# Optimization experiments

Measured on AMD Instinct MI355X. Metric: run time of the kernel, lower is better.

Reference implementation:

```python
import jax, jax.numpy as jnp
import numpy as np

BATCH, NUM_BSS, NUM_USERS, M, N = 32, 8, 32, 128, 4
LAGR_ITERS = 8
PSEUDOINV_SVAL_THRESH = 1e-12


def herm(a):
    return 0.5 * (a + jnp.swapaxes(a, -1, -2).conj())


def setup_inputs() -> dict:
    key = jax.random.key(0)
    ks = jax.random.split(key, 7)
    v_re = jax.random.normal(ks[0], (BATCH, NUM_USERS, M, N), jnp.float32)
    v_im = jax.random.normal(ks[1], (BATCH, NUM_USERS, M, N), jnp.float32)
    H_re = jax.random.normal(ks[2], (NUM_BSS, NUM_USERS, N, M), jnp.float32)
    H_im = jax.random.normal(ks[3], (NUM_BSS, NUM_USERS, N, M), jnp.float32)
    noise_pow = jax.random.uniform(ks[4], (BATCH, NUM_USERS), jnp.float32, 0.05, 1.0)
    rweights = jax.random.uniform(ks[5], (BATCH, NUM_USERS), jnp.float32, 0.1, 1.0)
    bss_pow = jnp.ones((BATCH, NUM_BSS), jnp.float32)
    assign = jax.random.randint(ks[6], (NUM_USERS,), 0, NUM_BSS).astype(jnp.int32)
    return {"v_re": v_re, "v_im": v_im, "H_re": H_re, "H_im": H_im,
            "noise_pow": noise_pow, "rweights": rweights, "bss_pow": bss_pow,
            "assign": assign}


def reference(v_re, v_im, H_re, H_im, noise_pow, rweights, bss_pow, assign):
    V = v_re + 1j * v_im          # [B,K,M,N] precoders
    H = H_re + 1j * H_im          # [C,K,N,M] channel BS c -> user k
    K = V.shape[1]
    C = H.shape[0]
    Ndim = V.shape[-1]
    eyeN = jnp.eye(Ndim, dtype=V.dtype)

    # Hg[j, i] = channel from assigned-BS-of-user-j to user i
    Hg = H[assign]                                    # [K,K,N,M]
    # downlink covariance per user i: noise*I + sum_j (H[bs_j,i] V_j)(.)^H
    HV = jnp.einsum('jinm,bjmp->bijnp', Hg, V)        # [B,Ki,Kj,N,N]
    cov = jnp.einsum('bijnp,bijqp->binq', HV, HV.conj())
    cov = herm(cov + noise_pow[..., None, None] * eyeN)
    icov = herm(jnp.linalg.inv(cov))                  # [B,K,N,N]

    idx = jnp.arange(K)
    Hd = Hg[idx, idx]                                 # [K,N,M] direct channels
    HdV = jnp.einsum('knm,bkmp->bknp', Hd, V)         # [B,K,N,N]
    u = jnp.einsum('bknq,bkqp->bknp', icov, HdV)      # receive filters
    w_inv = herm(eyeN - jnp.einsum('bkqn,bkqp->bknp', u.conj(), HdV))
    w = herm(jnp.linalg.inv(w_inv))                   # MSE weights (w_poly=None)
    uwu = herm(jnp.einsum('bknp,bkpq,bkrq->bknr', u, w, u.conj()))
    # v_tilde = H_ii^H u w * rate_weight
    vt = jnp.einsum('knm,bknp,bkpq->bkmq', Hd.conj(), u, w) * rweights[..., None, None]

    # uplink covariance per BS c: sum_k rw_k * H[c,k]^H uwu_k H[c,k]
    ul = herm(jnp.einsum('cknm,bkno,ckop,bk->bcmp', H.conj(), uwu, H, rweights))

    # aux per BS: sum over assigned users of v_tilde v_tilde^H
    Q = jnp.einsum('bkmn,bkpn->bkmp', vt, vt.conj())  # [B,K,M,M]
    aux = jnp.moveaxis(
        jax.ops.segment_sum(jnp.moveaxis(Q, 1, 0), assign, num_segments=C), 0, 1)  # [B,C,M,M]

    lam, E = jnp.linalg.eigh(ul)                      # [B,C,M], [B,C,M,M]
    lam = jnp.maximum(lam, 0.0)
    c = jnp.maximum(jnp.einsum('bcmi,bcmp,bcpi->bci', E.conj(), aux, E).real, 0.0)
    c = c / bss_pow[..., None]

    # solve sum_i c_i/(lam_i+mu)^2 = 1 for mu >= 0 by bisection in [0, sqrt(sum c)]
    hi = jnp.sqrt(jnp.sum(c, -1))
    lo = jnp.zeros_like(hi)
    for _ in range(LAGR_ITERS):
        mid = 0.5 * (lo + hi)
        f = jnp.sum(c / jnp.square(lam + mid[..., None] + 1e-20), -1)
        gt = f > 1.0
        lo = jnp.where(gt, mid, lo)
        hi = jnp.where(gt, hi, mid)
    mu = jnp.maximum(0.5 * (lo + hi), 0.0)            # [B,C]

    # pseudo-inverse of loaded UL covariance via its eigendecomposition
    lam_l = lam + mu[..., None]
    lam_l = jnp.where(lam_l < PSEUDOINV_SVAL_THRESH, 1e12, lam_l)
    inv_aug = herm(jnp.einsum('bcmi,bci,bcni->bcmn', E, 1.0 / lam_l, E.conj()))

    # v update: v_k = inv_aug[assign_k] @ v_tilde_k
    v_out = jnp.einsum('bkmp,bkpn->bkmn', inv_aug[:, assign], vt)  # [B,K,M,N]
    return v_out
```

## Files before the change

### kernel.cpp

```cpp
#include <hip/hip_runtime.h>

#define B_ 32
#define C_ 8
#define K_ 32
#define NCMAX 96
#define BSTR 129

__device__ __forceinline__ float2 cmul(float2 a, float2 b) {
  return make_float2(a.x*b.x - a.y*b.y, a.x*b.y + a.y*b.x);
}
__device__ __forceinline__ float2 cmulc(float2 a, float2 b) {
  return make_float2(a.x*b.x + a.y*b.y, a.y*b.x - a.x*b.y);
}
__device__ __forceinline__ float2 cadd(float2 a, float2 b){ return make_float2(a.x+b.x, a.y+b.y); }
__device__ __forceinline__ float2 csub(float2 a, float2 b){ return make_float2(a.x-b.x, a.y-b.y); }
__device__ __forceinline__ int SK(int r){ return r + ((r >> 3) << 1); }

template<int C>
__device__ __forceinline__ float dppadd(float x) {
  return x + __int_as_float(__builtin_amdgcn_update_dpp(
      0, __float_as_int(x), C, 0xF, 0xF, true));
}
__device__ __forceinline__ float bcast63(float x) {
  return __int_as_float(__builtin_amdgcn_readlane(__float_as_int(x), 63));
}
__device__ __forceinline__ float red4f(float x) {
  x = dppadd<0xB1>(x); return dppadd<0x4E>(x);
}
__device__ __forceinline__ float red16f(float x) {
  x = dppadd<0xB1>(x); x = dppadd<0x4E>(x);
  x = dppadd<0x141>(x); x = dppadd<0x140>(x);
  return x;
}
__device__ __forceinline__ float red64u(float x) {
  x = red16f(x);
  x = dppadd<0x142>(x);
  x = dppadd<0x143>(x);
  return bcast63(x);
}
__device__ __forceinline__ float2 red16c(float2 a){ a.x = red16f(a.x); a.y = red16f(a.y); return a; }
__device__ __forceinline__ float2 red64cu(float2 a){ a.x = red64u(a.x); a.y = red64u(a.y); return a; }

__device__ void herm4_inv(float2 a[4][4], float2 out[4][4]) {
  float idg[4];
  for (int j = 0; j < 4; ++j) {
    float d = sqrtf(fmaxf(a[j][j].x, 1e-30f));
    float id = 1.f / d;
    idg[j] = id;
    a[j][j] = make_float2(d, 0.f);
    for (int r = j+1; r < 4; ++r) { a[r][j].x *= id; a[r][j].y *= id; }
    for (int c = j+1; c < 4; ++c)
      for (int r = c; r < 4; ++r)
        a[r][c] = csub(a[r][c], cmulc(a[r][j], a[c][j]));
  }
  float2 li[4][4];
  for (int j = 0; j < 4; ++j) {
    li[j][j] = make_float2(idg[j], 0.f);
    for (int r = j+1; r < 4; ++r) {
      float2 s = make_float2(0.f, 0.f);
      for (int d = j; d < r; ++d) s = cadd(s, cmul(a[r][d], li[d][j]));
      li[r][j] = make_float2(-s.x*idg[r], -s.y*idg[r]);
    }
  }
  for (int p = 0; p < 4; ++p)
    for (int q = 0; q < 4; ++q) {
      float2 s = make_float2(0.f, 0.f);
      for (int d = (p > q ? p : q); d < 4; ++d)
        s = cadd(s, cmulc(li[d][q], li[d][p]));
      out[p][q] = s;
    }
}

__global__ __launch_bounds__(512, 1) void k_fused(
    const float* __restrict__ v_re, const float* __restrict__ v_im,
    const float* __restrict__ H_re, const float* __restrict__ H_im,
    const float* __restrict__ noise_pow, const float* __restrict__ rweights,
    const float* __restrict__ bss_pow, const int* __restrict__ assign_g,
    void* __restrict__ outp, int omode)
{
  const int t = threadIdx.x;
  const int lane = t & 63, wid = t >> 6;
  const int blk = blockIdx.x;
  const int b = blk >> 3, c = blk & 7;
  const int tm = t >> 4, tp = t & 15;
  const int rbase = tm * 4, cbase = tp * 8;

  __shared__ __align__(16) float2 BsL[NCMAX * BSTR];
  __shared__ __align__(16) float2 Arena[4224];
  __shared__ __align__(16) float2 pS[1024];
  __shared__ __align__(16) float2 wS[160];
  __shared__ __align__(16) float2 colS[160];
  __shared__ __align__(16) float2 pvS[128];
  __shared__ __align__(16) float2 tauS[128];
  __shared__ float dS[128], eS[128], cpS[128];
  __shared__ float red[8];
  __shared__ int asg[K_], ulist[K_], nc_s;

  float2* Wall = pS;
  float2* uwS  = pS + 512;
  float2* covS = Arena + 2576;
  float2* HdVS = Arena + 3088;
  float2* Tsc  = Arena;
  float2* Vp   = Arena;

  if (t < K_) asg[t] = assign_g[t];
  if (t == 0) {
    int n2 = 0;
    for (int k = 0; k < K_; ++k) if (assign_g[k] == c) ulist[n2++] = k;
    nc_s = n2;
  }
  {
    const int k = t >> 4, n = (t >> 2) & 3, q = t & 3;
    covS[t] = make_float2((n == q) ? noise_pow[b*K_ + k] : 0.f, 0.f);
  }
  __syncthreads();
  const int nc = nc_s;
  if (nc == 0) return;
  const int cols = 4 * nc;
  const int passes = (cols + 31) >> 5;

  {
    const int pn = t >> 2, qt = t & 3;
    const int kk = pn >> 2, nn = pn & 3;
    float2* Tb0 = Arena + 1552;
    float2* Tb1 = Arena + 2064;
    for (int j = 0; j < K_; j += 2) {
      #pragma unroll
      for (int bf = 0; bf < 2; ++bf) {
        const int vb = (b*K_ + j + bf) * 512;
        Arena[bf*776 + (t >> 2)*6 + (t & 3) + (t >> 7)*2] =
            make_float2(v_re[vb + t], v_im[vb + t]);
      }
      __syncthreads();
      float2 rr[2][4];
      #pragma unroll
      for (int bf = 0; bf < 2; ++bf) {
        const float2* Vq = Arena + bf*776 + qt*2;
        const int hb = ((asg[j + bf]*K_ + kk)*4 + nn) * 128;
        float2 a0 = {0,0}, a1 = {0,0}, a2 = {0,0}, a3 = {0,0};
        for (int m4 = qt*32; m4 < qt*32 + 32; m4 += 4) {
          const float4 hre = *(const float4*)&H_re[hb + m4];
          const float4 him = *(const float4*)&H_im[hb + m4];
          const float hx[4] = {hre.x, hre.y, hre.z, hre.w};
          const float hy[4] = {him.x, him.y, him.z, him.w};
          #pragma unroll
          for (int i2 = 0; i2 < 4; ++i2) {
            const float4 v01 = *(const float4*)&Vq[(m4 + i2)*6];
            const float4 v23 = *(const float4*)&Vq[(m4 + i2)*6 + 2];
            a0.x += hx[i2]*v01.x - hy[i2]*v01.y; a0.y += hx[i2]*v01.y + hy[i2]*v01.x;
            a1.x += hx[i2]*v01.z - hy[i2]*v01.w; a1.y += hx[i2]*v01.w + hy[i2]*v01.z;
            a2.x += hx[i2]*v23.x - hy[i2]*v23.y; a2.y += hx[i2]*v23.y + hy[i2]*v23.x;
            a3.x += hx[i2]*v23.z - hy[i2]*v23.w; a3.y += hx[i2]*v23.w + hy[i2]*v23.z;
          }
        }
        rr[bf][0] = a0; rr[bf][1] = a1; rr[bf][2] = a2; rr[bf][3] = a3;
      }
      #pragma unroll
      for (int bf = 0; bf < 2; ++bf)
        #pragma unroll
        for (int p = 0; p < 4; ++p) {
          rr[bf][p].x = red4f(rr[bf][p].x);
          rr[bf][p].y = red4f(rr[bf][p].y);
        }
      if (qt == 0) {
        #pragma unroll
        for (int p = 0; p < 4; ++p) {
          Tb0[pn*4 + p] = rr[0][p];
          Tb1[pn*4 + p] = rr[1][p];
        }
      }
      __syncthreads();
      {
        const int k2 = t >> 4, n2 = (t >> 2) & 3, q2 = t & 3;
        float2 acc = covS[t];
        #pragma unroll
        for (int p = 0; p < 4; ++p)
          acc = cadd(acc, cmulc(Tb0[(k2*4 + n2)*4 + p], Tb0[(k2*4 + q2)*4 + p]));
        #pragma unroll
        for (int p = 0; p < 4; ++p)
          acc = cadd(acc, cmulc(Tb1[(k2*4 + n2)*4 + p], Tb1[(k2*4 + q2)*4 + p]));
        covS[t] = acc;
        if (k2 == j)     HdVS[k2*16 + n2*4 + q2] = Tb0[(k2*4 + n2)*4 + q2];
        if (k2 == j + 1) HdVS[k2*16 + n2*4 + q2] = Tb1[(k2*4 + n2)*4 + q2];
      }
      __syncthreads();
    }
  }

  if (t < K_) {
    const int k = t;
    float2 a[4][4], ic[4][4], hv[4][4], u[4][4], wi[4][4], w[4][4], uw[4][4], W[4][4];
    const float rwk = rweights[b*K_ + k];
    for (int r = 0; r < 4; ++r)
      for (int c2 = 0; c2 < 4; ++c2) a[r][c2] = covS[k*16 + r*4 + c2];
    herm4_inv(a, ic);
    for (int r = 0; r < 4; ++r)
      for (int c2 = 0; c2 < 4; ++c2) hv[r][c2] = HdVS[k*16 + r*4 + c2];
    for (int n = 0; n < 4; ++n)
      for (int p = 0; p < 4; ++p) {
        float2 s = {0,0};
        for (int q = 0; q < 4; ++q) s = cadd(s, cmul(ic[n][q], hv[q][p]));
        u[n][p] = s;
      }
    for (int n = 0; n < 4; ++n)
      for (int p = 0; p < 4; ++p) {
        float2 s = make_float2((n == p) ? 1.f : 0.f, 0.f);
        for (int q = 0; q < 4; ++q) s = csub(s, cmulc(hv[q][p], u[q][n]));
        wi[n][p] = s;
      }
    herm4_inv(wi, w);
    for (int n = 0; n < 4; ++n)
      for (int q = 0; q < 4; ++q) {
        float2 s = {0,0};
        for (int p = 0; p < 4; ++p) s = cadd(s, cmul(u[n][p], w[p][q]));
        uw[n][q] = s;
      }
    for (int n = 0; n < 4; ++n)
      for (int r = 0; r < 4; ++r) {
        float2 s = {0,0};
        for (int q = 0; q < 4; ++q) s = cadd(s, cmulc(uw[n][q], u[r][q]));
        W[n][r] = make_float2(s.x * rwk, s.y * rwk);
      }
    for (int n = 0; n < 4; ++n)
      for (int r = n; r < 4; ++r) {
        float2 x1 = W[n][r], x2 = W[r][n];
        float2 hm = make_float2(0.5f*(x1.x + x2.x), 0.5f*(x1.y - x2.y));
        W[n][r] = hm; W[r][n] = make_float2(hm.x, -hm.y);
      }
    for (int idx = 0; idx < 16; ++idx) {
      uwS[k*16 + idx]  = uw[idx >> 2][idx & 3];
      Wall[k*16 + idx] = W[idx >> 2][idx & 3];
    }
  }
  __syncthreads();

  float2 Areg[4][8];
  #pragma unroll
  for (int j = 0; j < 4; ++j)
    #pragma unroll
    for (int cc = 0; cc < 8; ++cc) Areg[j][cc] = make_float2(0.f, 0.f);
  for (int k = 0; k < K_; k += 2) {
    #pragma unroll
    for (int bf = 0; bf < 2; ++bf) {
      const int hb = (c*K_ + k + bf) * 512;
      Arena[bf*520 + (t >> 7)*130 + (t & 127)] = make_float2(H_re[hb + t], H_im[hb + t]);
    }
    __syncthreads();
    #pragma unroll
    for (int bf = 0; bf < 2; ++bf) {
      const int n = t >> 7, p = t & 127;
      const float2* HsB = Arena + bf*520;
      const int kb = (k + bf)*16 + n*4;
      float2 y = {0,0};
      #pragma unroll
      for (int o = 0; o < 4; ++o) y = cadd(y, cmul(Wall[kb + o], HsB[o*130 + p]));
      Arena[1040 + bf*640 + n*160 + p + ((p >> 3) << 1)] = y;
    }
    __syncthreads();
    #pragma unroll
    for (int bf = 0; bf < 2; ++bf) {
      const float2* HsB = Arena + bf*520;
      const float2* YsB = Arena + 1040 + bf*640;
      #pragma unroll
      for (int n = 0; n < 4; ++n) {
        const float4 ha = *(const float4*)&HsB[n*130 + rbase];
        const float4 hc = *(const float4*)&HsB[n*130 + rbase + 2];
        const float2 h0 = make_float2(ha.x, ha.y), h1 = make_float2(ha.z, ha.w);
        const float2 h2 = make_float2(hc.x, hc.y), h3 = make_float2(hc.z, hc.w);
        const float2* yb = &YsB[n*160 + tp*10];
        #pragma unroll
        for (int hq = 0; hq < 2; ++hq) {
          float2 y[4];
          #pragma unroll
          for (int a2 = 0; a2 < 4; a2 += 2) {
            const float4 y4 = *(const float4*)&yb[hq*4 + a2];
            y[a2] = make_float2(y4.x, y4.y); y[a2+1] = make_float2(y4.z, y4.w);
          }
          #pragma unroll
          for (int c4 = 0; c4 < 4; ++c4) {
            const int cc = hq*4 + c4;
            Areg[0][cc].x += h0.x*y[c4].x + h0.y*y[c4].y;
            Areg[0][cc].y += h0.x*y[c4].y - h0.y*y[c4].x;
            Areg[1][cc].x += h1.x*y[c4].x + h1.y*y[c4].y;
            Areg[1][cc].y += h1.x*y[c4].y - h1.y*y[c4].x;
            Areg[2][cc].x += h2.x*y[c4].x + h2.y*y[c4].y;
            Areg[2][cc].y += h2.x*y[c4].y - h2.y*y[c4].x;
            Areg[3][cc].x += h3.x*y[c4].x + h3.y*y[c4].y;
            Areg[3][cc].y += h3.x*y[c4].y - h3.y*y[c4].x;
          }
        }
      }
    }
    __syncthreads();
  }

  float2 Bw0[8], Bw1[8];
  #pragma unroll
  for (int qq = 0; qq < 8; ++qq) { Bw0[qq] = make_float2(0.f,0.f); Bw1[qq] = make_float2(0.f,0.f); }
  float trp = 0.f;
  #pragma unroll
  for (int qq = 0; qq < 8; ++qq) {
    const int col = wid + 8*qq;
    if (col < cols) {
      const int slot = col >> 2, qn = col & 3;
      const int k = ulist[slot];
      const float rwk = rweights[b*K_ + k];
      const int hb = (c*K_ + k) * 512;
      float2 a0 = {0,0}, a1 = {0,0};
      #pragma unroll
      for (int n = 0; n < 4; ++n) {
        const float2 uwv = uwS[k*16 + n*4 + qn];
        a0 = cadd(a0, cmulc(uwv, make_float2(H_re[hb + n*128 + lane],
                                             H_im[hb + n*128 + lane])));
        a1 = cadd(a1, cmulc(uwv, make_float2(H_re[hb + n*128 + lane + 64],
                                             H_im[hb + n*128 + lane + 64])));
      }
      a0.x *= rwk; a0.y *= rwk; a1.x *= rwk; a1.y *= rwk;
      Bw0[qq] = a0; Bw1[qq] = a1;
      trp += a0.x*a0.x + a0.y*a0.y + a1.x*a1.x + a1.y*a1.y;
    }
  }
  trp = red64u(trp);
  if (lane == 0) red[wid] = trp;
  __syncthreads();
  const float inv_bss = 1.f / bss_pow[b*C_ + c];
  float hi = sqrtf((red[0] + red[1] + red[2] + red[3] +
                    red[4] + red[5] + red[6] + red[7]) * inv_bss);
  float lo = 0.f;

  if (tp == 0) {
    #pragma unroll
    for (int j = 0; j < 4; ++j) colS[SK(rbase + j)] = Areg[j][0];
  }
  __syncthreads();

  #pragma unroll 1
  for (int i = 0; i < 127; ++i) {
    float2 vr[4], vc[8], v0, v1, tau, sc;
    {
      const float2 x0 = colS[SK(lane)], x1 = colS[SK(lane + 64)];
      float sig = 0.f;
      if (lane >= i + 2)      sig += x0.x*x0.x + x0.y*x0.y;
      if (lane + 64 >= i + 2) sig += x1.x*x1.x + x1.y*x1.y;
      sig = red64u(sig);
      const float2 al = colS[SK(i + 1)];
      float beta;
      if (sig <= 1e-30f && fabsf(al.y) <= 1e-30f) {
        beta = al.x; tau = make_float2(0.f, 0.f); sc = make_float2(0.f, 0.f);
      } else {
        const float mag = sqrtf(al.x*al.x + al.y*al.y + sig);
        beta = (al.x >= 0.f) ? -mag : mag;
        const float ib = 1.f / beta;
        tau = make_float2((beta - al.x) * ib, -al.y * ib);
        const float dx = al.x - beta, dy = al.y;
        const float dn = 1.f / (dx*dx + dy*dy);
        sc = make_float2(dx*dn, -dy*dn);
      }
      if (t == 0) { eS[i] = beta; tauS[i] = tau; }
      v0 = (lane <= i) ? make_float2(0.f,0.f)
         : (lane == i + 1 ? make_float2(1.f,0.f) : cmul(x0, sc));
      { const int r1 = lane + 64;
        v1 = (r1 <= i) ? make_float2(0.f,0.f)
           : (r1 == i + 1 ? make_float2(1.f,0.f) : cmul(x1, sc)); }
      #pragma unroll
      for (int j = 0; j < 4; ++j) {
        const int r = rbase + j;
        const float2 x = colS[SK(r)];
        vr[j] = (r <= i) ? make_float2(0.f, 0.f)
              : (r == i + 1 ? make_float2(1.f, 0.f) : cmul(x, sc));
      }
      {
        const int cb = SK(cbase);
        const float4 c01 = *(const float4*)&colS[cb];
        const float4 c23 = *(const float4*)&colS[cb + 2];
        const float4 c45 = *(const float4*)&colS[cb + 4];
        const float4 c67 = *(const float4*)&colS[cb + 6];
        const float2 cx[8] = { make_float2(c01.x,c01.y), make_float2(c01.z,c01.w),
                               make_float2(c23.x,c23.y), make_float2(c23.z,c23.w),
                               make_float2(c45.x,c45.y), make_float2(c45.z,c45.w),
                               make_float2(c67.x,c67.y), make_float2(c67.z,c67.w) };
        #pragma unroll
        for (int cc = 0; cc < 8; ++cc) {
          const int r = cbase + cc;
          vc[cc] = (r <= i) ? make_float2(0.f, 0.f)
                 : (r == i + 1 ? make_float2(1.f, 0.f) : cmul(cx[cc], sc));
        }
      }
    }
    {
      float2 part[4];
      #pragma unroll
      for (int j = 0; j < 4; ++j) {
        float2 s = cmul(Areg[j][0], vc[0]);
        #pragma unroll
        for (int cc = 1; cc < 8; ++cc) s = cadd(s, cmul(Areg[j][cc], vc[cc]));
        part[j] = s;
      }
      #pragma unroll
      for (int j = 0; j < 4; ++j) part[j] = red16c(part[j]);
      #pragma unroll
      for (int j = 0; j < 4; ++j) if (tp == j) pvS[rbase + j] = part[j];
      const float2 tauc = make_float2(tau.x, -tau.y);
      #pragma unroll
      for (int qq = 0; qq < 8; ++qq) {
        const int col = wid + 8*qq;
        if (col >= cols) continue;
        float2 d = cadd(cmulc(Bw0[qq], v0), cmulc(Bw1[qq], v1));
        d = red64cu(d);
        const float2 dBt = cmul(tauc, d);
        Bw0[qq] = csub(Bw0[qq], cmul(dBt, v0));
        Bw1[qq] = csub(Bw1[qq], cmul(dBt, v1));
      }
    }
    __syncthreads();

    if (wid == 0) {
      float2 p0 = {0.f,0.f}, p1 = {0.f,0.f};
      if (lane > i)      p0 = cmul(tau, pvS[lane]);
      if (lane + 64 > i) p1 = cmul(tau, pvS[lane + 64]);
      float2 d0 = cadd(cmulc(p0, v0), cmulc(p1, v1));
      d0 = red64cu(d0);
      const float alr = -0.5f * (tau.x*d0.x + tau.y*d0.y);
      wS[SK(lane)]      = cadd(p0, make_float2(alr*v0.x, alr*v0.y));
      wS[SK(lane + 64)] = cadd(p1, make_float2(alr*v1.x, alr*v1.y));
    }
    __syncthreads();

    {
      float2 wr[4], wc[8];
      #pragma unroll
      for (int j = 0; j < 4; ++j) wr[j] = wS[SK(rbase + j)];
      {
        const int cb = SK(cbase);
        const float4 w01 = *(const float4*)&wS[cb];
        const float4 w23 = *(const float4*)&wS[cb + 2];
        const float4 w45 = *(const float4*)&wS[cb + 4];
        const float4 w67 = *(const float4*)&wS[cb + 6];
        wc[0] = make_float2(w01.x,w01.y); wc[1] = make_float2(w01.z,w01.w);
        wc[2] = make_float2(w23.x,w23.y); wc[3] = make_float2(w23.z,w23.w);
        wc[4] = make_float2(w45.x,w45.y); wc[5] = make_float2(w45.z,w45.w);
        wc[6] = make_float2(w67.x,w67.y); wc[7] = make_float2(w67.z,w67.w);
      }
      #pragma unroll
      for (int j = 0; j < 4; ++j)
        #pragma unroll
        for (int cc = 0; cc < 8; ++cc)
          Areg[j][cc] = csub(Areg[j][cc], cadd(cmulc(vr[j], wc[cc]), cmulc(wr[j], vc[cc])));
      if (tp == (i >> 3)) {
        #pragma unroll
        for (int cc = 0; cc < 8; ++cc) if (cc == (i & 7)) {
          #pragma unroll
          for (int j = 0; j < 4; ++j) if (rbase + j >= i + 1) Areg[j][cc] = vr[j];
        }
      }
      if (tp == ((i + 1) >> 3)) {
        #pragma unroll
        for (int cc = 0; cc < 8; ++cc) if (cc == ((i + 1) & 7)) {
          #pragma unroll
          for (int j = 0; j < 4; ++j) colS[SK(rbase + j)] = Areg[j][cc];
        }
      }
    }
    __syncthreads();
  }

  if (tp == (tm >> 1)) {
    const int co = (tm & 1) * 4;
    #pragma unroll
    for (int j = 0; j < 4; ++j)
      #pragma unroll
      for (int cc = 0; cc < 8; ++cc)
        if (cc == co + j) dS[rbase + j] = Areg[j][cc].x;
  }
  #pragma unroll
  for (int qq = 0; qq < 8; ++qq) {
    const int col = wid + 8*qq;
    if (col < cols) {
      BsL[col*BSTR + lane]      = Bw0[qq];
      BsL[col*BSTR + lane + 64] = Bw1[qq];
    }
  }
  __syncthreads();

  if (wid == 0) {
    for (int it = 0; it <= 8; ++it) {
      const float mu = 0.5f * (lo + hi);
      float fsum = 0.f;
      for (int p = 0; p < passes; ++p) {
        const int colg = 32*p + (lane & 31);
        const bool act = (lane < 32) && (colg < cols);
        float2* Bcol = BsL + colg*BSTR;
        float m = dS[0] + mu;
        float im = 1.f / m;
        float2 g = act ? Bcol[0] : make_float2(0.f, 0.f);
        g.x *= im; g.y *= im;
        if (act) Tsc[lane] = g;
        float cp = eS[0] * im;
        if (lane == 0) cpS[0] = cp;
        #pragma unroll 4
        for (int r = 1; r < 128; ++r) {
          const float e0 = eS[r-1];
          m = dS[r] + mu - e0 * cp;
          im = 1.f / m;
          float2 gr = act ? Bcol[r] : make_float2(0.f, 0.f);
          gr.x = (gr.x - e0 * g.x) * im;
          gr.y = (gr.y - e0 * g.y) * im;
          g = gr;
          if (act) Tsc[r*33 + lane] = gr;
          if (r < 127) { cp = eS[r] * im; if (lane == 0) cpS[r] = cp; }
        }
        float2 z = g;
        float acc = z.x*z.x + z.y*z.y;
        if (it == 8 && act) Bcol[127] = z;
        #pragma unroll 4
        for (int r = 126; r >= 0; --r) {
          const float cpr = cpS[r];
          const float2 gp = act ? Tsc[r*33 + lane] : make_float2(0.f, 0.f);
          z.x = gp.x - cpr * z.x;
          z.y = gp.y - cpr * z.y;
          acc += z.x*z.x + z.y*z.y;
          if (it == 8 && act) Bcol[r] = z;
        }
        if (act) fsum += acc;
      }
      if (it < 8) {
        fsum = red64u(fsum);
        const float f = fsum * inv_bss;
        if (f > 1.0f) lo = mu; else hi = mu;
      }
    }
  }
  __syncthreads();

  for (int base = 0; base < cols; base += 32) {
    float2 z0[4], z1[4];
    bool act[4];
    #pragma unroll
    for (int qq = 0; qq < 4; ++qq) {
      const int col = base + wid + 8*qq;
      act[qq] = (col < cols);
      const int cc2 = act[qq] ? col : 0;
      z0[qq] = BsL[cc2*BSTR + lane];
      z1[qq] = BsL[cc2*BSTR + lane + 64];
    }
    for (int P = 7; P >= 0; --P) {
      const int p0i = P * 16;
      const int smax = (P == 7) ? 14 : 15;
      __syncthreads();
      if (tp == 2*P) {
        #pragma unroll
        for (int s = 0; s < 8; ++s) {
          const int ii = p0i + s;
          #pragma unroll
          for (int j = 0; j < 4; ++j) {
            const int r = rbase + j;
            Vp[(s << 7) + r] = (r >= ii + 1) ? Areg[j][s] : make_float2(0.f, 0.f);
          }
        }
      }
      if (tp == 2*P + 1) {
        #pragma unroll
        for (int s = 8; s < 16; ++s) {
          if (s > smax) continue;
          const int ii = p0i + s;
          #pragma unroll
          for (int j = 0; j < 4; ++j) {
            const int r = rbase + j;
            Vp[(s << 7) + r] = (r >= ii + 1) ? Areg[j][s - 8] : make_float2(0.f, 0.f);
          }
        }
      }
      __syncthreads();
      for (int s = smax; s >= 0; --s) {
        const float2 tv = tauS[p0i + s];
        const float2 v0b = Vp[(s << 7) + lane];
        const float2 v1b = Vp[(s << 7) + lane + 64];
        float2 d[4];
        #pragma unroll
        for (int qq = 0; qq < 4; ++qq) {
          d[qq] = cadd(cmulc(z0[qq], v0b), cmulc(z1[qq], v1b));
          d[qq] = red64cu(d[qq]);
        }
        #pragma unroll
        for (int qq = 0; qq < 4; ++qq) {
          const float2 td = cmul(tv, d[qq]);
          z0[qq] = csub(z0[qq], cmul(td, v0b));
          z1[qq] = csub(z1[qq], cmul(td, v1b));
        }
      }
    }
    #pragma unroll
    for (int qq = 0; qq < 4; ++qq) if (act[qq]) {
      const int col = base + wid + 8*qq;
      const int slotc = col >> 2, qn = col & 3;
      const int k = ulist[slotc];
      const size_t obase = (size_t)(b*K_ + k) * 512;
      const size_t oe0 = obase + (size_t)lane*4 + qn;
      const size_t oe1 = obase + (size_t)(lane + 64)*4 + qn;
      if (omode == 0) {
        ((float2*)outp)[oe0] = z0[qq];
        ((float2*)outp)[oe1] = z1[qq];
      } else {
        ((float*)outp)[oe0] = z0[qq].x;
        ((float*)outp)[oe1] = z1[qq].x;
      }
    }
  }
}

extern "C" void kernel_launch(void* const* d_in, const int* in_sizes, int n_in,
                              void* d_out, int out_size, void* d_ws, size_t ws_size,
                              hipStream_t stream)
{
  (void)in_sizes; (void)n_in; (void)d_ws; (void)ws_size;
  const float* v_re   = (const float*)d_in[0];
  const float* v_im   = (const float*)d_in[1];
  const float* H_re   = (const float*)d_in[2];
  const float* H_im   = (const float*)d_in[3];
  const float* noise  = (const float*)d_in[4];
  const float* rw     = (const float*)d_in[5];
  const float* bss    = (const float*)d_in[6];
  const int*   assign = (const int*)d_in[7];

  const int omode = (out_size == B_*K_*128*4) ? 1 : 0;

  hipLaunchKernelGGL(k_fused, dim3(B_*C_), dim3(512), 0, stream,
                     v_re, v_im, H_re, H_im, noise, rw, bss, assign, d_out, omode);
}
```

Measured before the change: 1.181 ms.

## Split tridiagonal bisection solves across two waves and drop w broadcast barrier

The bisection solve over batched tridiagonal systems now splits its column passes between two wavefronts instead of one. Each wave gets its own scratch (the second uses spare BsL space) and the waves combine partial sums through shared memory with barriers. In the Householder update loop, every thread now computes the w vector entries it needs from pvS, which removes one wS store and its __syncthreads per reflector step. The cost is redundant arithmetic per thread, extra barriers per bisection iteration, and a dependence on the BsL region past column 64 being free.

```diff
diff --git a/kernel.cpp b/kernel.cpp
--- a/kernel.cpp
+++ b/kernel.cpp
@@ -88,11 +88,10 @@
   __shared__ __align__(16) float2 BsL[NCMAX * BSTR];
   __shared__ __align__(16) float2 Arena[4224];
   __shared__ __align__(16) float2 pS[1024];
-  __shared__ __align__(16) float2 wS[160];
   __shared__ __align__(16) float2 colS[160];
-  __shared__ __align__(16) float2 pvS[128];
+  __shared__ __align__(16) float2 pvS[160];
   __shared__ __align__(16) float2 tauS[128];
-  __shared__ float dS[128], eS[128], cpS[128];
+  __shared__ float dS[128], eS[128], cpS[128], cpS2[128];
   __shared__ float red[8];
   __shared__ int asg[K_], ulist[K_], nc_s;
 
@@ -399,7 +398,7 @@
       #pragma unroll
       for (int j = 0; j < 4; ++j) part[j] = red16c(part[j]);
       #pragma unroll
-      for (int j = 0; j < 4; ++j) if (tp == j) pvS[rbase + j] = part[j];
+      for (int j = 0; j < 4; ++j) if (tp == j) pvS[SK(rbase + j)] = part[j];
       const float2 tauc = make_float2(tau.x, -tau.y);
       #pragma unroll
       for (int qq = 0; qq < 8; ++qq) {
@@ -414,38 +413,28 @@
     }
     __syncthreads();
 
-    if (wid == 0) {
-      float2 p0 = {0.f,0.f}, p1 = {0.f,0.f};
-      if (lane > i)      p0 = cmul(tau, pvS[lane]);
-      if (lane + 64 > i) p1 = cmul(tau, pvS[lane + 64]);
+    {
+      float2 p0 = (lane > i)      ? cmul(tau, pvS[SK(lane)])      : make_float2(0.f,0.f);
+      float2 p1 = (lane + 64 > i) ? cmul(tau, pvS[SK(lane + 64)]) : make_float2(0.f,0.f);
       float2 d0 = cadd(cmulc(p0, v0), cmulc(p1, v1));
       d0 = red64cu(d0);
       const float alr = -0.5f * (tau.x*d0.x + tau.y*d0.y);
-      wS[SK(lane)]      = cadd(p0, make_float2(alr*v0.x, alr*v0.y));
-      wS[SK(lane + 64)] = cadd(p1, make_float2(alr*v1.x, alr*v1.y));
-    }
-    __syncthreads();
-
-    {
-      float2 wr[4], wc[8];
-      #pragma unroll
-      for (int j = 0; j < 4; ++j) wr[j] = wS[SK(rbase + j)];
-      {
-        const int cb = SK(cbase);
-        const float4 w01 = *(const float4*)&wS[cb];
-        const float4 w23 = *(const float4*)&wS[cb + 2];
-        const float4 w45 = *(const float4*)&wS[cb + 4];
-        const float4 w67 = *(const float4*)&wS[cb + 6];
-        wc[0] = make_float2(w01.x,w01.y); wc[1] = make_float2(w01.z,w01.w);
-        wc[2] = make_float2(w23.x,w23.y); wc[3] = make_float2(w23.z,w23.w);
-        wc[4] = make_float2(w45.x,w45.y); wc[5] = make_float2(w45.z,w45.w);
-        wc[6] = make_float2(w67.x,w67.y); wc[7] = make_float2(w67.z,w67.w);
-      }
-      #pragma unroll
-      for (int j = 0; j < 4; ++j)
-        #pragma unroll
-        for (int cc = 0; cc < 8; ++cc)
-          Areg[j][cc] = csub(Areg[j][cc], cadd(cmulc(vr[j], wc[cc]), cmulc(wr[j], vc[cc])));
+      float2 wr[4];
+      #pragma unroll
+      for (int j = 0; j < 4; ++j) {
+        const int r = rbase + j;
+        float2 p = (r > i) ? cmul(tau, pvS[SK(r)]) : make_float2(0.f,0.f);
+        wr[j] = make_float2(p.x + alr*vr[j].x, p.y + alr*vr[j].y);
+      }
+      #pragma unroll
+      for (int cc = 0; cc < 8; ++cc) {
+        const int r = cbase + cc;
+        float2 p = (r > i) ? cmul(tau, pvS[SK(r)]) : make_float2(0.f,0.f);
+        const float2 wcv = make_float2(p.x + alr*vc[cc].x, p.y + alr*vc[cc].y);
+        #pragma unroll
+        for (int j = 0; j < 4; ++j)
+          Areg[j][cc] = csub(Areg[j][cc], cadd(cmulc(vr[j], wcv), cmulc(wr[j], vc[cc])));
+      }
       if (tp == (i >> 3)) {
         #pragma unroll
         for (int cc = 0; cc < 8; ++cc) if (cc == (i & 7)) {
@@ -482,55 +471,63 @@
   }
   __syncthreads();
 
-  if (wid == 0) {
+  {
+    const int bw = (passes > 1) ? 2 : 1;
+    float2* myT = (wid == 0) ? Tsc : (BsL + 64*BSTR);
+    float*  myCp = (wid == 0) ? cpS : cpS2;
+    const int TS = (wid == 0) ? 33 : 32;
     for (int it = 0; it <= 8; ++it) {
       const float mu = 0.5f * (lo + hi);
       float fsum = 0.f;
-      for (int p = 0; p < passes; ++p) {
-        const int colg = 32*p + (lane & 31);
-        const bool act = (lane < 32) && (colg < cols);
-        float2* Bcol = BsL + colg*BSTR;
-        float m = dS[0] + mu;
-        float im = 1.f / m;
-        float2 g = act ? Bcol[0] : make_float2(0.f, 0.f);
-        g.x *= im; g.y *= im;
-        if (act) Tsc[lane] = g;
-        float cp = eS[0] * im;
-        if (lane == 0) cpS[0] = cp;
-        #pragma unroll 4
-        for (int r = 1; r < 128; ++r) {
-          const float e0 = eS[r-1];
-          m = dS[r] + mu - e0 * cp;
-          im = 1.f / m;
-          float2 gr = act ? Bcol[r] : make_float2(0.f, 0.f);
-          gr.x = (gr.x - e0 * g.x) * im;
-          gr.y = (gr.y - e0 * g.y) * im;
-          g = gr;
-          if (act) Tsc[r*33 + lane] = gr;
-          if (r < 127) { cp = eS[r] * im; if (lane == 0) cpS[r] = cp; }
-        }
-        float2 z = g;
-        float acc = z.x*z.x + z.y*z.y;
-        if (it == 8 && act) Bcol[127] = z;
-        #pragma unroll 4
-        for (int r = 126; r >= 0; --r) {
-          const float cpr = cpS[r];
-          const float2 gp = act ? Tsc[r*33 + lane] : make_float2(0.f, 0.f);
-          z.x = gp.x - cpr * z.x;
-          z.y = gp.y - cpr * z.y;
-          acc += z.x*z.x + z.y*z.y;
-          if (it == 8 && act) Bcol[r] = z;
-        }
-        if (act) fsum += acc;
-      }
+      if (wid < bw) {
+        for (int p = wid; p < passes; p += bw) {
+          const int colg = 32*p + (lane & 31);
+          const bool act = (lane < 32) && (colg < cols);
+          float2* Bcol = BsL + colg*BSTR;
+          float m = dS[0] + mu;
+          float im = 1.f / m;
+          float2 g = act ? Bcol[0] : make_float2(0.f, 0.f);
+          g.x *= im; g.y *= im;
+          if (act) myT[lane] = g;
+          float cp = eS[0] * im;
+          if (lane == 0) myCp[0] = cp;
+          #pragma unroll 4
+          for (int r = 1; r < 128; ++r) {
+            const float e0 = eS[r-1];
+            m = dS[r] + mu - e0 * cp;
+            im = 1.f / m;
+            float2 gr = act ? Bcol[r] : make_float2(0.f, 0.f);
+            gr.x = (gr.x - e0 * g.x) * im;
+            gr.y = (gr.y - e0 * g.y) * im;
+            g = gr;
+            if (act) myT[r*TS + lane] = gr;
+            if (r < 127) { cp = eS[r] * im; if (lane == 0) myCp[r] = cp; }
+          }
+          float2 z = g;
+          float acc = z.x*z.x + z.y*z.y;
+          if (it == 8 && act) Bcol[127] = z;
+          #pragma unroll 4
+          for (int r = 126; r >= 0; --r) {
+            const float cpr = myCp[r];
+            const float2 gp = act ? myT[r*TS + lane] : make_float2(0.f, 0.f);
+            z.x = gp.x - cpr * z.x;
+            z.y = gp.y - cpr * z.y;
+            acc += z.x*z.x + z.y*z.y;
+            if (it == 8 && act) Bcol[r] = z;
+          }
+          if (act) fsum += acc;
+        }
+      }
+      fsum = red64u(fsum);
+      if (lane == 0) red[wid] = fsum;
+      __syncthreads();
       if (it < 8) {
-        fsum = red64u(fsum);
-        const float f = fsum * inv_bss;
+        const float f = (red[0] + red[1]) * inv_bss;
         if (f > 1.0f) lo = mu; else hi = mu;
       }
-    }
-  }
-  __syncthreads();
+      __syncthreads();
+    }
+  }
 
   for (int base = 0; base < cols; base += 32) {
     float2 z0[4], z1[4];
```

Measured after the change: 1.238 ms. +4.8%, slower.
